# Kernel optimization log

Measured on AMD Instinct MI355X. Metric: run time of the kernel, lower is better.

Reference implementation:

```python
import jax, jax.numpy as jnp
import numpy as np

LN_EPS = 1e-5


def _ln(x, g, b):
    m = x.mean(-1, keepdims=True)
    v = ((x - m) ** 2).mean(-1, keepdims=True)
    return (x - m) * jax.lax.rsqrt(v + LN_EPS) * g + b


def setup_inputs() -> dict:
    key = jax.random.key(0)
    ks = jax.random.split(key, 16)
    B, K, D_IN, DM, DF, L = 16384, 32, 4, 64, 128, 2
    Nx, Ny, Nt = 128, 128, 64
    N = Nx * Ny * Nt
    s = 0.05
    inp = {
        "q_lin_idx": jax.random.randint(ks[0], (B,), 0, N),
        "offsets_ijk": jax.random.randint(ks[1], (K, 3), 0, 5),
        "vals": jax.random.normal(ks[2], (N,), dtype=jnp.float32),
        "coords": jax.random.normal(ks[3], (N, 3), dtype=jnp.float32),
        "grid_scales": jax.random.uniform(ks[4], (3,), dtype=jnp.float32),
        "Nx": Nx, "Ny": Ny, "Nt": Nt,
        "log_gammas": jnp.zeros((3,), jnp.float32),
        "Wp": jax.random.normal(ks[5], (DM, D_IN)) * s,
        "bp": jnp.zeros((DM,)),
        "Wqkv": jax.random.normal(ks[6], (L, 3 * DM, DM)) * s,
        "bqkv": jnp.zeros((L, 3 * DM)),
        "Wo": jax.random.normal(ks[7], (L, DM, DM)) * s,
        "bo": jnp.zeros((L, DM)),
        "W1": jax.random.normal(ks[8], (L, DF, DM)) * s,
        "b1": jnp.zeros((L, DF)),
        "W2": jax.random.normal(ks[9], (L, DM, DF)) * s,
        "b2": jnp.zeros((L, DM)),
        "ln1_g": jnp.ones((L, DM)), "ln1_b": jnp.zeros((L, DM)),
        "ln2_g": jnp.ones((L, DM)), "ln2_b": jnp.zeros((L, DM)),
        "hg": jnp.ones((DM,)), "hb": jnp.zeros((DM,)),
        "hW1": jax.random.normal(ks[10], (DM, DM)) * s,
        "hb1": jnp.zeros((DM,)),
        "hW2": jax.random.normal(ks[11], (1, DM)) * s,
        "hb2": jnp.zeros((1,)),
    }
    return inp


def reference(q_lin_idx, offsets_ijk, vals, coords, grid_scales, Nx, Ny, Nt,
              log_gammas, Wp, bp, Wqkv, bqkv, Wo, bo, W1, b1, W2, b2,
              ln1_g, ln1_b, ln2_g, ln2_b, hg, hb, hW1, hb1, hW2, hb2):
    # --- periodic neighbor gather ---
    NyNt = Ny * Nt
    i = q_lin_idx // NyNt
    r = q_lin_idx % NyNt
    j = r // Nt
    k0 = r % Nt
    di, dj, dk = offsets_ijk[:, 0], offsets_ijk[:, 1], offsets_ijk[:, 2]
    I = (i[:, None] + di[None, :]) % Nx
    J = (j[:, None] + dj[None, :]) % Ny
    Kc = (k0[:, None] + dk[None, :]) % Nt
    nb_lin = I * NyNt + J * Nt + Kc            # (B, K)

    B, K = nb_lin.shape
    rel = offsets_ijk.astype(jnp.float32) * grid_scales * jnp.exp(log_gammas)  # (K, 3)
    nb_vals = vals[nb_lin][..., None]          # (B, K, 1) irregular gather
    tokens = jnp.concatenate([jnp.broadcast_to(rel, (B, K, 3)), nb_vals], axis=-1)

    # --- input projection ---
    h = tokens @ Wp.T + bp                     # (B, K, 64)
    DM = Wp.shape[0]
    H = 4
    Dh = DM // H

    # --- 2-layer post-norm transformer encoder (eval mode, dropout off) ---
    for l in range(Wqkv.shape[0]):
        qkv = h @ Wqkv[l].T + bqkv[l]
        q_, k_, v_ = jnp.split(qkv, 3, axis=-1)
        q_ = q_.reshape(B, K, H, Dh)
        k_ = k_.reshape(B, K, H, Dh)
        v_ = v_.reshape(B, K, H, Dh)
        scores = jnp.einsum('bqhd,bkhd->bhqk', q_, k_) / jnp.sqrt(jnp.float32(Dh))
        attn = jax.nn.softmax(scores, axis=-1)
        o = jnp.einsum('bhqk,bkhd->bqhd', attn, v_).reshape(B, K, DM)
        h = _ln(h + o @ Wo[l].T + bo[l], ln1_g[l], ln1_b[l])
        ff = jax.nn.relu(h @ W1[l].T + b1[l]) @ W2[l].T + b2[l]
        h = _ln(h + ff, ln2_g[l], ln2_b[l])

    # --- mean pool + head ---
    hm = h.mean(axis=1)
    z = _ln(hm, hg, hb)
    z = jax.nn.gelu(z @ hW1.T + hb1, approximate=False)
    out = (z @ hW2.T + hb2)[:, 0]              # (B,)
    return out
```

## Files before the change

### kernel.cpp

```cpp
#include <hip/hip_runtime.h>
#include <math.h>

#define KTOK  32
#define DM    64
#define DH    16
#define NH    4
#define DFF   128
#define KVSTR 36

__global__ __launch_bounds__(64, 2)
void ff_kernel(
    const int*   __restrict__ qidx,
    const int*   __restrict__ offs,
    const float* __restrict__ vals,
    const float* __restrict__ gscale,
    const int*   __restrict__ NxP,
    const int*   __restrict__ NyP,
    const int*   __restrict__ NtP,
    const float* __restrict__ lgam,
    const float* __restrict__ Wp,   const float* __restrict__ bp,
    const float* __restrict__ Wqkv, const float* __restrict__ bqkv,
    const float* __restrict__ Wo,   const float* __restrict__ bo,
    const float* __restrict__ W1w,  const float* __restrict__ b1w,
    const float* __restrict__ W2w,  const float* __restrict__ b2w,
    const float* __restrict__ ln1g, const float* __restrict__ ln1b,
    const float* __restrict__ ln2g, const float* __restrict__ ln2b,
    const float* __restrict__ hg,   const float* __restrict__ hb,
    const float* __restrict__ hW1,  const float* __restrict__ hb1,
    const float* __restrict__ hW2,  const float* __restrict__ hb2,
    float* __restrict__ out)
{
    __shared__ float kv[2][KTOK][KVSTR];

    const int tid = threadIdx.x;
    const int bl  = tid >> 5;
    const int kk  = tid & 31;
    const int b   = blockIdx.x * 2 + bl;

    const int Nx = NxP[0], Ny = NyP[0], Nt = NtP[0];
    const int NyNt = Ny * Nt;

    const int q  = qidx[b];
    const int i0 = q / NyNt;
    const int r0 = q - i0 * NyNt;
    const int j0 = r0 / Nt;
    const int t0 = r0 - j0 * Nt;

    const int di = offs[kk*3+0], dj = offs[kk*3+1], dk = offs[kk*3+2];
    int I = i0 + di; if (I >= Nx) I -= Nx;
    int J = j0 + dj; if (J >= Ny) J -= Ny;
    int Kc = t0 + dk; if (Kc >= Nt) Kc -= Nt;
    const float val = vals[I*NyNt + J*Nt + Kc];

    const float r1 = (float)di * gscale[0] * expf(lgam[0]);
    const float r2 = (float)dj * gscale[1] * expf(lgam[1]);
    const float r3 = (float)dk * gscale[2] * expf(lgam[2]);

    float h[DM];
#pragma unroll
    for (int d = 0; d < DM; ++d)
        h[d] = bp[d] + Wp[d*4+0]*r1 + Wp[d*4+1]*r2 + Wp[d*4+2]*r3 + Wp[d*4+3]*val;

    for (int l = 0; l < 2; ++l) {
        const float* Wq  = Wqkv + l*(3*DM)*DM;
        const float* bq  = bqkv + l*(3*DM);
        const float* WoL = Wo   + l*DM*DM;

        float xacc[DM];
#pragma unroll
        for (int dp = 0; dp < DM; ++dp) xacc[dp] = h[dp] + bo[l*DM+dp];

        for (int hh = 0; hh < NH; ++hh) {
            __syncthreads();

            for (int t = 0; t < DH; ++t) {
                const float* wk = Wq + (DM   + hh*DH + t)*DM;
                const float* wv = Wq + (2*DM + hh*DH + t)*DM;
                float ak0 = bq[DM+hh*DH+t],   ak1 = 0.f;
                float av0 = bq[2*DM+hh*DH+t], av1 = 0.f;
#pragma unroll
                for (int d = 0; d < DM; d += 2) {
                    ak0 = fmaf(h[d],   wk[d],   ak0);
                    ak1 = fmaf(h[d+1], wk[d+1], ak1);
                    av0 = fmaf(h[d],   wv[d],   av0);
                    av1 = fmaf(h[d+1], wv[d+1], av1);
                }
                kv[bl][kk][t]    = ak0 + ak1;
                kv[bl][kk][DH+t] = av0 + av1;
            }
            __syncthreads();

            float qh[DH];
#pragma unroll
            for (int t = 0; t < DH; ++t) {
                const float* wq = Wq + (hh*DH + t)*DM;
                float a0 = bq[hh*DH + t], a1 = 0.f;
#pragma unroll
                for (int d = 0; d < DM; d += 2) {
                    a0 = fmaf(h[d],   wq[d],   a0);
                    a1 = fmaf(h[d+1], wq[d+1], a1);
                }
                qh[t] = (a0 + a1) * 0.25f;
            }

            float sc[KTOK];
            float mx = -1e30f;
#pragma unroll
            for (int kx = 0; kx < KTOK; ++kx) {
                const float4* kr = (const float4*)&kv[bl][kx][0];
                float s0 = 0.f, s1 = 0.f;
#pragma unroll
                for (int t4 = 0; t4 < 4; ++t4) {
                    float4 k4 = kr[t4];
                    s0 = fmaf(qh[t4*4+0], k4.x, s0);
                    s1 = fmaf(qh[t4*4+1], k4.y, s1);
                    s0 = fmaf(qh[t4*4+2], k4.z, s0);
                    s1 = fmaf(qh[t4*4+3], k4.w, s1);
                }
                sc[kx] = s0 + s1;
                mx = fmaxf(mx, sc[kx]);
            }
            float den = 0.f;
#pragma unroll
            for (int kx = 0; kx < KTOK; ++kx) {
                float e = expf(sc[kx] - mx);
                sc[kx] = e; den += e;
            }
            const float inv = 1.f / den;

            float oh[DH];
#pragma unroll
            for (int t = 0; t < DH; ++t) oh[t] = 0.f;
#pragma unroll
            for (int kx = 0; kx < KTOK; ++kx) {
                const float w = sc[kx] * inv;
                const float4* vr = (const float4*)&kv[bl][kx][DH];
#pragma unroll
                for (int t4 = 0; t4 < 4; ++t4) {
                    float4 v4 = vr[t4];
                    oh[t4*4+0] = fmaf(w, v4.x, oh[t4*4+0]);
                    oh[t4*4+1] = fmaf(w, v4.y, oh[t4*4+1]);
                    oh[t4*4+2] = fmaf(w, v4.z, oh[t4*4+2]);
                    oh[t4*4+3] = fmaf(w, v4.w, oh[t4*4+3]);
                }
            }

#pragma unroll
            for (int dp = 0; dp < DM; ++dp) {
                const float* w = WoL + dp*DM + hh*DH;
                float s0 = 0.f, s1 = 0.f;
#pragma unroll
                for (int t = 0; t < DH; t += 2) {
                    s0 = fmaf(oh[t],   w[t],   s0);
                    s1 = fmaf(oh[t+1], w[t+1], s1);
                }
                xacc[dp] += s0 + s1;
            }
        }

        {
            float mean = 0.f;
#pragma unroll
            for (int dp = 0; dp < DM; ++dp) mean += xacc[dp];
            mean *= (1.f/DM);
            float var = 0.f;
#pragma unroll
            for (int dp = 0; dp < DM; ++dp) { float dx = xacc[dp]-mean; var = fmaf(dx,dx,var); }
            var *= (1.f/DM);
            const float rs = rsqrtf(var + 1e-5f);
#pragma unroll
            for (int dp = 0; dp < DM; ++dp)
                h[dp] = (xacc[dp]-mean)*rs*ln1g[l*DM+dp] + ln1b[l*DM+dp];
        }

        float a2[DM];
#pragma unroll
        for (int dp = 0; dp < DM; ++dp) a2[dp] = h[dp] + b2w[l*DM+dp];
        const float* W1L = W1w + l*DFF*DM;
        const float* W2L = W2w + l*DM*DFF;
        for (int f0 = 0; f0 < DFF; f0 += 8) {
            float a[8];
#pragma unroll
            for (int fc = 0; fc < 8; ++fc) {
                const float* w1 = W1L + (f0+fc)*DM;
                float s0 = b1w[l*DFF+f0+fc], s1 = 0.f;
#pragma unroll
                for (int d = 0; d < DM; d += 2) {
                    s0 = fmaf(h[d],   w1[d],   s0);
                    s1 = fmaf(h[d+1], w1[d+1], s1);
                }
                a[fc] = fmaxf(s0 + s1, 0.f);
            }
#pragma unroll
            for (int dp = 0; dp < DM; ++dp) {
                const float* w2 = W2L + dp*DFF + f0;
                float t0 = fmaf(a[0], w2[0], fmaf(a[1], w2[1], fmaf(a[2], w2[2], a[3]*w2[3])));
                float t1 = fmaf(a[4], w2[4], fmaf(a[5], w2[5], fmaf(a[6], w2[6], a[7]*w2[7])));
                a2[dp] += t0 + t1;
            }
        }

        {
            float mean = 0.f;
#pragma unroll
            for (int dp = 0; dp < DM; ++dp) mean += a2[dp];
            mean *= (1.f/DM);
            float var = 0.f;
#pragma unroll
            for (int dp = 0; dp < DM; ++dp) { float dx = a2[dp]-mean; var = fmaf(dx,dx,var); }
            var *= (1.f/DM);
            const float rs = rsqrtf(var + 1e-5f);
#pragma unroll
            for (int dp = 0; dp < DM; ++dp)
                h[dp] = (a2[dp]-mean)*rs*ln2g[l*DM+dp] + ln2b[l*DM+dp];
        }
    }

    float hm[DM];
#pragma unroll
    for (int d = 0; d < DM; ++d) {
        float v = h[d];
        v += __shfl_xor(v, 1,  64);
        v += __shfl_xor(v, 2,  64);
        v += __shfl_xor(v, 4,  64);
        v += __shfl_xor(v, 8,  64);
        v += __shfl_xor(v, 16, 64);
        hm[d] = v * (1.f/KTOK);
    }
    {
        float mean = 0.f;
#pragma unroll
        for (int d = 0; d < DM; ++d) mean += hm[d];
        mean *= (1.f/DM);
        float var = 0.f;
#pragma unroll
        for (int d = 0; d < DM; ++d) { float dx = hm[d]-mean; var = fmaf(dx,dx,var); }
        var *= (1.f/DM);
        const float rs = rsqrtf(var + 1e-5f);
#pragma unroll
        for (int d = 0; d < DM; ++d)
            hm[d] = (hm[d]-mean)*rs*hg[d] + hb[d];
    }

    float acc = 0.f;
#pragma unroll
    for (int zz = 0; zz < 2; ++zz) {
        const int zi = kk + zz*32;
        const float4* w4 = (const float4*)(hW1 + zi*DM);
        float a0 = hb1[zi], a1 = 0.f;
#pragma unroll
        for (int d4 = 0; d4 < DM/4; ++d4) {
            float4 w = w4[d4];
            a0 = fmaf(hm[d4*4+0], w.x, a0);
            a1 = fmaf(hm[d4*4+1], w.y, a1);
            a0 = fmaf(hm[d4*4+2], w.z, a0);
            a1 = fmaf(hm[d4*4+3], w.w, a1);
        }
        const float a = a0 + a1;
        const float g = 0.5f * a * (1.f + erff(a * 0.70710678118654752f));
        acc = fmaf(g, hW2[zi], acc);
    }
    acc += __shfl_xor(acc, 1,  64);
    acc += __shfl_xor(acc, 2,  64);
    acc += __shfl_xor(acc, 4,  64);
    acc += __shfl_xor(acc, 8,  64);
    acc += __shfl_xor(acc, 16, 64);

    if (kk == 0) out[b] = acc + hb2[0];
}

extern "C" void kernel_launch(void* const* d_in, const int* in_sizes, int n_in,
                              void* d_out, int out_size, void* d_ws, size_t ws_size,
                              hipStream_t stream) {
    const int*   qidx   = (const int*)  d_in[0];
    const int*   offs   = (const int*)  d_in[1];
    const float* vals   = (const float*)d_in[2];
    const float* gscale = (const float*)d_in[4];
    const int*   NxP    = (const int*)  d_in[5];
    const int*   NyP    = (const int*)  d_in[6];
    const int*   NtP    = (const int*)  d_in[7];
    const float* lgam   = (const float*)d_in[8];
    const float* Wp     = (const float*)d_in[9];
    const float* bp     = (const float*)d_in[10];
    const float* Wqkv   = (const float*)d_in[11];
    const float* bqkv   = (const float*)d_in[12];
    const float* Wo     = (const float*)d_in[13];
    const float* bo     = (const float*)d_in[14];
    const float* W1w    = (const float*)d_in[15];
    const float* b1w    = (const float*)d_in[16];
    const float* W2w    = (const float*)d_in[17];
    const float* b2w    = (const float*)d_in[18];
    const float* ln1g   = (const float*)d_in[19];
    const float* ln1b   = (const float*)d_in[20];
    const float* ln2g   = (const float*)d_in[21];
    const float* ln2b   = (const float*)d_in[22];
    const float* hg     = (const float*)d_in[23];
    const float* hb     = (const float*)d_in[24];
    const float* hW1    = (const float*)d_in[25];
    const float* hb1    = (const float*)d_in[26];
    const float* hW2    = (const float*)d_in[27];
    const float* hb2    = (const float*)d_in[28];
    float* outp = (float*)d_out;

    const int B = in_sizes[0];
    dim3 grid(B / 2), block(64);
    hipLaunchKernelGGL(ff_kernel, grid, block, 0, stream,
        qidx, offs, vals, gscale, NxP, NyP, NtP, lgam,
        Wp, bp, Wqkv, bqkv, Wo, bo, W1w, b1w, W2w, b2w,
        ln1g, ln1b, ln2g, ln2b, hg, hb, hW1, hb1, hW2, hb2, outp);
}
```

Measured before the change: 2.320 ms.

## Stage per-head and FFN weight tiles in shared memory across 8 queries per block

Blocks grow from 2 to 8 queries (256 threads). Each head's Q/K/V/Wo weight slice and each 32-wide chunk of W1/W2 is staged cooperatively into a 16 KB shared buffer, and the dot products read it as float4. This replaces per-thread scalar global and L1 weight loads with shared-memory reads reused by 8 queries. In exchange it adds extra block barriers per head and per FFN chunk, and the larger shared footprint and block size may limit occupancy.

```diff
diff --git a/kernel.cpp b/kernel.cpp
--- a/kernel.cpp
+++ b/kernel.cpp
@@ -7,8 +7,9 @@
 #define NH    4
 #define DFF   128
 #define KVSTR 36
-
-__global__ __launch_bounds__(64, 2)
+#define QB    8
+
+__global__ __launch_bounds__(256, 2)
 void ff_kernel(
     const int*   __restrict__ qidx,
     const int*   __restrict__ offs,
@@ -30,12 +31,13 @@
     const float* __restrict__ hW2,  const float* __restrict__ hb2,
     float* __restrict__ out)
 {
-    __shared__ float kv[2][KTOK][KVSTR];
-
-    const int tid = threadIdx.x;
-    const int bl  = tid >> 5;
-    const int kk  = tid & 31;
-    const int b   = blockIdx.x * 2 + bl;
+    __shared__ float kv[QB][KTOK][KVSTR];
+    __shared__ float wbig[4096];
+
+    const int tid   = threadIdx.x;
+    const int qslot = tid >> 5;
+    const int kk    = tid & 31;
+    const int b     = blockIdx.x * QB + qslot;
 
     const int Nx = NxP[0], Ny = NyP[0], Nt = NtP[0];
     const int NyNt = Ny * Nt;
@@ -73,32 +75,49 @@
         for (int hh = 0; hh < NH; ++hh) {
             __syncthreads();
 
+            {
+                float4* dst = (float4*)wbig;
+                dst[tid]       = ((const float4*)(Wq + (hh*DH)*DM       ))[tid];
+                dst[256 + tid] = ((const float4*)(Wq + (DM   + hh*DH)*DM))[tid];
+                dst[512 + tid] = ((const float4*)(Wq + (2*DM + hh*DH)*DM))[tid];
+                dst[768 + tid] = *(const float4*)(WoL + (tid>>2)*DM + hh*DH + (tid&3)*4);
+            }
+            __syncthreads();
+
             for (int t = 0; t < DH; ++t) {
-                const float* wk = Wq + (DM   + hh*DH + t)*DM;
-                const float* wv = Wq + (2*DM + hh*DH + t)*DM;
+                const float4* wk4 = (const float4*)(wbig + 1024 + t*DM);
+                const float4* wv4 = (const float4*)(wbig + 2048 + t*DM);
                 float ak0 = bq[DM+hh*DH+t],   ak1 = 0.f;
                 float av0 = bq[2*DM+hh*DH+t], av1 = 0.f;
 #pragma unroll
-                for (int d = 0; d < DM; d += 2) {
-                    ak0 = fmaf(h[d],   wk[d],   ak0);
-                    ak1 = fmaf(h[d+1], wk[d+1], ak1);
-                    av0 = fmaf(h[d],   wv[d],   av0);
-                    av1 = fmaf(h[d+1], wv[d+1], av1);
-                }
-                kv[bl][kk][t]    = ak0 + ak1;
-                kv[bl][kk][DH+t] = av0 + av1;
+                for (int d4 = 0; d4 < 16; ++d4) {
+                    float4 wk = wk4[d4], wv = wv4[d4];
+                    ak0 = fmaf(h[d4*4+0], wk.x, ak0);
+                    ak1 = fmaf(h[d4*4+1], wk.y, ak1);
+                    ak0 = fmaf(h[d4*4+2], wk.z, ak0);
+                    ak1 = fmaf(h[d4*4+3], wk.w, ak1);
+                    av0 = fmaf(h[d4*4+0], wv.x, av0);
+                    av1 = fmaf(h[d4*4+1], wv.y, av1);
+                    av0 = fmaf(h[d4*4+2], wv.z, av0);
+                    av1 = fmaf(h[d4*4+3], wv.w, av1);
+                }
+                kv[qslot][kk][t]    = ak0 + ak1;
+                kv[qslot][kk][DH+t] = av0 + av1;
             }
             __syncthreads();
 
             float qh[DH];
 #pragma unroll
             for (int t = 0; t < DH; ++t) {
-                const float* wq = Wq + (hh*DH + t)*DM;
+                const float4* wq4 = (const float4*)(wbig + t*DM);
                 float a0 = bq[hh*DH + t], a1 = 0.f;
 #pragma unroll
-                for (int d = 0; d < DM; d += 2) {
-                    a0 = fmaf(h[d],   wq[d],   a0);
-                    a1 = fmaf(h[d+1], wq[d+1], a1);
+                for (int d4 = 0; d4 < 16; ++d4) {
+                    float4 w = wq4[d4];
+                    a0 = fmaf(h[d4*4+0], w.x, a0);
+                    a1 = fmaf(h[d4*4+1], w.y, a1);
+                    a0 = fmaf(h[d4*4+2], w.z, a0);
+                    a1 = fmaf(h[d4*4+3], w.w, a1);
                 }
                 qh[t] = (a0 + a1) * 0.25f;
             }
@@ -107,7 +126,7 @@
             float mx = -1e30f;
 #pragma unroll
             for (int kx = 0; kx < KTOK; ++kx) {
-                const float4* kr = (const float4*)&kv[bl][kx][0];
+                const float4* kr = (const float4*)&kv[qslot][kx][0];
                 float s0 = 0.f, s1 = 0.f;
 #pragma unroll
                 for (int t4 = 0; t4 < 4; ++t4) {
@@ -134,7 +153,7 @@
 #pragma unroll
             for (int kx = 0; kx < KTOK; ++kx) {
                 const float w = sc[kx] * inv;
-                const float4* vr = (const float4*)&kv[bl][kx][DH];
+                const float4* vr = (const float4*)&kv[qslot][kx][DH];
 #pragma unroll
                 for (int t4 = 0; t4 < 4; ++t4) {
                     float4 v4 = vr[t4];
@@ -147,13 +166,17 @@
 
 #pragma unroll
             for (int dp = 0; dp < DM; ++dp) {
-                const float* w = WoL + dp*DM + hh*DH;
+                const float4* w4 = (const float4*)(wbig + 3072 + dp*DH);
+                float4 wa = w4[0], wb = w4[1], wc = w4[2], wd = w4[3];
                 float s0 = 0.f, s1 = 0.f;
-#pragma unroll
-                for (int t = 0; t < DH; t += 2) {
-                    s0 = fmaf(oh[t],   w[t],   s0);
-                    s1 = fmaf(oh[t+1], w[t+1], s1);
-                }
+                s0 = fmaf(oh[0],  wa.x, s0); s1 = fmaf(oh[1],  wa.y, s1);
+                s0 = fmaf(oh[2],  wa.z, s0); s1 = fmaf(oh[3],  wa.w, s1);
+                s0 = fmaf(oh[4],  wb.x, s0); s1 = fmaf(oh[5],  wb.y, s1);
+                s0 = fmaf(oh[6],  wb.z, s0); s1 = fmaf(oh[7],  wb.w, s1);
+                s0 = fmaf(oh[8],  wc.x, s0); s1 = fmaf(oh[9],  wc.y, s1);
+                s0 = fmaf(oh[10], wc.z, s0); s1 = fmaf(oh[11], wc.w, s1);
+                s0 = fmaf(oh[12], wd.x, s0); s1 = fmaf(oh[13], wd.y, s1);
+                s0 = fmaf(oh[14], wd.z, s0); s1 = fmaf(oh[15], wd.w, s1);
                 xacc[dp] += s0 + s1;
             }
         }
@@ -178,25 +201,44 @@
         for (int dp = 0; dp < DM; ++dp) a2[dp] = h[dp] + b2w[l*DM+dp];
         const float* W1L = W1w + l*DFF*DM;
         const float* W2L = W2w + l*DM*DFF;
-        for (int f0 = 0; f0 < DFF; f0 += 8) {
-            float a[8];
-#pragma unroll
-            for (int fc = 0; fc < 8; ++fc) {
-                const float* w1 = W1L + (f0+fc)*DM;
-                float s0 = b1w[l*DFF+f0+fc], s1 = 0.f;
-#pragma unroll
-                for (int d = 0; d < DM; d += 2) {
-                    s0 = fmaf(h[d],   w1[d],   s0);
-                    s1 = fmaf(h[d+1], w1[d+1], s1);
-                }
-                a[fc] = fmaxf(s0 + s1, 0.f);
-            }
-#pragma unroll
-            for (int dp = 0; dp < DM; ++dp) {
-                const float* w2 = W2L + dp*DFF + f0;
-                float t0 = fmaf(a[0], w2[0], fmaf(a[1], w2[1], fmaf(a[2], w2[2], a[3]*w2[3])));
-                float t1 = fmaf(a[4], w2[4], fmaf(a[5], w2[5], fmaf(a[6], w2[6], a[7]*w2[7])));
-                a2[dp] += t0 + t1;
+        for (int f0 = 0; f0 < DFF; f0 += 32) {
+            __syncthreads();
+            {
+                float4* dst = (float4*)wbig;
+                const float4* s1p = (const float4*)(W1L + f0*DM);
+                dst[tid]       = s1p[tid];
+                dst[256 + tid] = s1p[256 + tid];
+                int g = tid;
+                dst[512 + g] = *(const float4*)(W2L + (g>>3)*DFF + f0 + (g&7)*4);
+                g = tid + 256;
+                dst[512 + g] = *(const float4*)(W2L + (g>>3)*DFF + f0 + (g&7)*4);
+            }
+            __syncthreads();
+
+            for (int fc0 = 0; fc0 < 32; fc0 += 8) {
+                float a[8];
+#pragma unroll
+                for (int fc = 0; fc < 8; ++fc) {
+                    const float4* w14 = (const float4*)(wbig + (fc0+fc)*DM);
+                    float s0 = b1w[l*DFF + f0 + fc0 + fc], s1 = 0.f;
+#pragma unroll
+                    for (int d4 = 0; d4 < 16; ++d4) {
+                        float4 w = w14[d4];
+                        s0 = fmaf(h[d4*4+0], w.x, s0);
+                        s1 = fmaf(h[d4*4+1], w.y, s1);
+                        s0 = fmaf(h[d4*4+2], w.z, s0);
+                        s1 = fmaf(h[d4*4+3], w.w, s1);
+                    }
+                    a[fc] = fmaxf(s0 + s1, 0.f);
+                }
+#pragma unroll
+                for (int dp = 0; dp < DM; ++dp) {
+                    const float4* w24 = (const float4*)(wbig + 2048 + dp*32 + fc0);
+                    float4 wa = w24[0], wb = w24[1];
+                    float u0 = fmaf(a[0], wa.x, fmaf(a[1], wa.y, fmaf(a[2], wa.z, a[3]*wa.w)));
+                    float u1 = fmaf(a[4], wb.x, fmaf(a[5], wb.y, fmaf(a[6], wb.z, a[7]*wb.w)));
+                    a2[dp] += u0 + u1;
+                }
             }
         }
 
@@ -303,7 +345,7 @@
     float* outp = (float*)d_out;
 
     const int B = in_sizes[0];
-    dim3 grid(B / 2), block(64);
+    dim3 grid(B / QB), block(256);
     hipLaunchKernelGGL(ff_kernel, grid, block, 0, stream,
         qidx, offs, vals, gscale, NxP, NyP, NtP, lgam,
         Wp, bp, Wqkv, bqkv, Wo, bo, W1w, b1w, W2w, b2w,
```

New measurement: 3.761 ms. 1.62x slower.
